# Kernel tuning notes

Measured on AMD Instinct MI355X. Metric: run time of the kernel, lower is better.

The kernel has to match this reference:

```python
import jax, jax.numpy as jnp
import numpy as np

B = 16384
S0, S1 = 7, 7
NB, NC = 2, 20
WC, WN = 5.0, 0.5  # weight_coord, weight_noobject
D = NB * 5 + NC  # 30


def setup_inputs() -> dict:
    key = jax.random.key(0)
    k1, k2, k3, k4 = jax.random.split(key, 4)
    predication = jax.random.normal(k1, (B, S0 * S1 * D), dtype=jnp.float32)
    grid = jax.random.randint(k2, (B, S0, S1), 0, 2, dtype=jnp.int32)
    tbox = jax.random.uniform(k3, (B, S0, S1, 4), dtype=jnp.float32)
    # keep target w,h strictly positive (real boxes), offsets in [0,1)
    tbox = tbox.at[..., 2:].set(0.05 + 0.9 * tbox[..., 2:])
    tcls = jax.random.randint(k4, (B, S0, S1), 0, NC, dtype=jnp.int32)
    return {"predication": predication, "grid": grid, "tbox": tbox, "tcls": tcls}


def _yolo_loss(predication, grid, tbox, tcls):
    pred = predication.reshape(B, S0, S1, D)
    conf = jax.nn.sigmoid(pred[..., :NB])                                  # (B,S0,S1,NB)
    pb = jax.nn.sigmoid(pred[..., NB:5 * NB]).reshape(B, S0, S1, NB, 4)    # (B,S0,S1,NB,4)
    cls = jax.nn.softmax(pred[..., 5 * NB:], axis=-1)                      # (B,S0,S1,NC)

    # cell coordinates: x = column index, y = row index (matches the [1,0] swap in torch code)
    xg = jnp.arange(S1, dtype=pred.dtype)[None, None, :]   # (1,1,S1)
    yg = jnp.arange(S0, dtype=pred.dtype)[None, :, None]   # (1,S0,1)

    tox, toy, tw, th = tbox[..., 0], tbox[..., 1], tbox[..., 2], tbox[..., 3]
    tcx = (xg + tox) / S0
    tcy = (yg + toy) / S1

    pcx = (xg[..., None] + pb[..., 0]) / S0   # (B,S0,S1,NB)
    pcy = (yg[..., None] + pb[..., 1]) / S1
    pw, ph = pb[..., 2], pb[..., 3]

    # IOU of each predicted box vs the cell's target box (same formula as _calc_iou)
    tb_ = jnp.minimum(tcx[..., None] + tw[..., None] / 2, pcx + pw / 2) - \
          jnp.maximum(tcx[..., None] - tw[..., None] / 2, pcx - pw / 2)
    lr_ = jnp.minimum(tcy[..., None] + th[..., None] / 2, pcy + ph / 2) - \
          jnp.maximum(tcy[..., None] - th[..., None] / 2, pcy - ph / 2)
    inter = jnp.where((tb_ < 0) | (lr_ < 0), 0.0, tb_ * lr_)
    iou = inter / ((tw * th)[..., None] + pw * ph - inter)                 # (B,S0,S1,NB)

    # best predictor chosen on detached IOUs (original uses pred_boxes.detach())
    best = jnp.argmax(jax.lax.stop_gradient(iou), axis=-1)                 # (B,S0,S1)

    take = lambda a: jnp.take_along_axis(a, best[..., None], axis=-1)[..., 0]
    iou_b = take(iou)          # attached IOU re-used in confidence loss
    conf_b = take(conf)
    pbb = jnp.take_along_axis(pb, best[..., None, None], axis=3)[..., 0, :]  # (B,S0,S1,4)

    cls_t = jnp.take_along_axis(cls, tcls[..., None], axis=-1)[..., 0]

    coord = (pbb[..., 0] - tox) ** 2 + (pbb[..., 1] - toy) ** 2 \
          + (jnp.sqrt(pbb[..., 2]) - jnp.sqrt(tw)) ** 2 \
          + (jnp.sqrt(pbb[..., 3]) - jnp.sqrt(th)) ** 2

    obj_loss = WC * coord + (conf_b - iou_b) ** 2 + (1.0 - cls_t) ** 2     # (B,S0,S1)
    noobj_loss = WN * jnp.sum(conf ** 2, axis=-1)                          # (B,S0,S1)

    objm = (grid == 1).astype(pred.dtype)
    total = jnp.sum(objm * obj_loss + (1.0 - objm) * noobj_loss)
    return total / B


def reference(predication, grid, tbox, tcls):
    return _yolo_loss(predication, grid, tbox, tcls)
```

## Files before the change

### kernel.cpp

```cpp
#include <hip/hip_runtime.h>
#include <math.h>

namespace {

constexpr int kB    = 16384;
constexpr int kS0   = 7;
constexpr int kS1   = 7;
constexpr int kD    = 30;
constexpr int kCells = kB * kS0 * kS1;
constexpr int TPB   = 256;
constexpr int NBLK  = kCells / TPB;
constexpr float kInv7 = 1.0f / 7.0f;
constexpr float kWC = 5.0f;
constexpr float kWN = 0.5f;

__device__ __forceinline__ float frcp(float x) {
    return __builtin_amdgcn_rcpf(x);
}

__device__ __forceinline__ float sigm(float x) {
    return frcp(1.0f + __expf(-x));
}

__global__ void __launch_bounds__(TPB, 4) yolo_loss_kernel(
    const float* __restrict__ pred,
    const int*   __restrict__ grid,
    const float* __restrict__ tbox,
    const int*   __restrict__ tcls,
    float* __restrict__ partials)
{
    __shared__ float wsum[TPB / 64];

    const int tid  = threadIdx.x;
    const int cell = blockIdx.x * TPB + tid;
    const int wave = tid >> 6;
    const int lane = tid & 63;

    const float2* __restrict__ p2 =
        reinterpret_cast<const float2*>(pred + (size_t)cell * kD);

    float f[kD];
    #pragma unroll
    for (int q = 0; q < kD / 2; ++q) {
        const float2 t = p2[q];
        f[2 * q]     = t.x;
        f[2 * q + 1] = t.y;
    }

    const float4 tb4 = reinterpret_cast<const float4*>(tbox)[cell];
    const int g  = grid[cell];
    const int tc = tcls[cell];

    __builtin_amdgcn_sched_barrier(0);

    const int cj = cell % kS1;
    const int ci = (cell / kS1) % kS0;
    const float tox = tb4.x, toy = tb4.y, tw = tb4.z, th = tb4.w;

    const float conf0 = sigm(f[0]);
    const float conf1 = sigm(f[1]);
    float pbx[2], pby[2], pbw[2], pbh[2];
    #pragma unroll
    for (int k = 0; k < 2; ++k) {
        pbx[k] = sigm(f[2 + 4 * k + 0]);
        pby[k] = sigm(f[2 + 4 * k + 1]);
        pbw[k] = sigm(f[2 + 4 * k + 2]);
        pbh[k] = sigm(f[2 + 4 * k + 3]);
    }

    float csum = 0.0f, et = 0.0f;
    #pragma unroll
    for (int q = 0; q < 20; ++q) {
        const float e = __expf(f[10 + q]);
        csum += e;
        et = (q == tc) ? e : et;
    }
    const float cls_t = et * frcp(csum);

    const float x = (float)cj, y = (float)ci;
    const float tcx = (x + tox) * kInv7;
    const float tcy = (y + toy) * kInv7;
    const float thw = tw * 0.5f, thh = th * 0.5f;
    const float tarea = tw * th;

    float iou[2];
    #pragma unroll
    for (int k = 0; k < 2; ++k) {
        const float pcx = (x + pbx[k]) * kInv7;
        const float pcy = (y + pby[k]) * kInv7;
        const float pw = pbw[k], ph = pbh[k];
        const float tb_ = fminf(tcx + thw, pcx + pw * 0.5f) - fmaxf(tcx - thw, pcx - pw * 0.5f);
        const float lr_ = fminf(tcy + thh, pcy + ph * 0.5f) - fmaxf(tcy - thh, pcy - ph * 0.5f);
        float inter = tb_ * lr_;
        inter = (tb_ < 0.0f || lr_ < 0.0f) ? 0.0f : inter;
        iou[k] = inter * frcp(tarea + pw * ph - inter);
    }

    const bool b1 = (iou[1] > iou[0]);
    const float bx = b1 ? pbx[1] : pbx[0];
    const float by = b1 ? pby[1] : pby[0];
    const float bw = b1 ? pbw[1] : pbw[0];
    const float bh = b1 ? pbh[1] : pbh[0];
    const float conf_b = b1 ? conf1 : conf0;
    const float iou_b  = b1 ? iou[1] : iou[0];

    const float dx = bx - tox;
    const float dy = by - toy;
    const float dw = sqrtf(bw) - sqrtf(tw);
    const float dh = sqrtf(bh) - sqrtf(th);
    const float coord = dx * dx + dy * dy + dw * dw + dh * dh;
    const float d1 = conf_b - iou_b;
    const float d2 = 1.0f - cls_t;
    const float obj   = kWC * coord + d1 * d1 + d2 * d2;
    const float noobj = kWN * (conf0 * conf0 + conf1 * conf1);

    float v = (g == 1) ? obj : noobj;

    #pragma unroll
    for (int off = 32; off > 0; off >>= 1) v += __shfl_down(v, off, 64);
    if (lane == 0) wsum[wave] = v;
    __syncthreads();
    if (tid == 0) {
        partials[blockIdx.x] = wsum[0] + wsum[1] + wsum[2] + wsum[3];
    }
}

__global__ void __launch_bounds__(256) finish_kernel(
    const float* __restrict__ partials, float* __restrict__ out)
{
    __shared__ float wsum[4];
    const int tid = threadIdx.x;
    float v = 0.0f;
    for (int i = tid; i < NBLK; i += 256) v += partials[i];
    #pragma unroll
    for (int off = 32; off > 0; off >>= 1) v += __shfl_down(v, off, 64);
    if ((tid & 63) == 0) wsum[tid >> 6] = v;
    __syncthreads();
    if (tid == 0) out[0] = (wsum[0] + wsum[1] + wsum[2] + wsum[3]) * (1.0f / kB);
}

}

extern "C" void kernel_launch(void* const* d_in, const int* in_sizes, int n_in,
                              void* d_out, int out_size, void* d_ws, size_t ws_size,
                              hipStream_t stream) {
    const float* pred = (const float*)d_in[0];
    const int*   grid = (const int*)d_in[1];
    const float* tbox = (const float*)d_in[2];
    const int*   tcls = (const int*)d_in[3];
    float* out      = (float*)d_out;
    float* partials = (float*)d_ws;

    yolo_loss_kernel<<<NBLK, TPB, 0, stream>>>(pred, grid, tbox, tcls, partials);
    finish_kernel<<<1, 256, 0, stream>>>(partials, out);
}
```

Before: 159.8 us.

## Process four tiles per block with register double-buffered prefetch

Each block now handles four 256-cell tiles instead of one, prefetching the next tile's predictions and targets into a second register buffer while the current tile is computed. This cuts the block count and partial-sum count by four and aims to overlap global-load latency with the math. In exchange, register pressure roughly doubles and occupancy is lowered (launch bounds go from 4 to 3 blocks), which could weaken latency hiding in this memory-bound kernel.

```diff
diff --git a/kernel.cpp b/kernel.cpp
--- a/kernel.cpp
+++ b/kernel.cpp
@@ -9,7 +9,8 @@
 constexpr int kD    = 30;
 constexpr int kCells = kB * kS0 * kS1;
 constexpr int TPB   = 256;
-constexpr int NBLK  = kCells / TPB;
+constexpr int T     = 4;
+constexpr int NBLK  = kCells / (TPB * T);
 constexpr float kInv7 = 1.0f / 7.0f;
 constexpr float kWC = 5.0f;
 constexpr float kWN = 0.5f;
@@ -22,7 +23,7 @@
     return frcp(1.0f + __expf(-x));
 }
 
-__global__ void __launch_bounds__(TPB, 4) yolo_loss_kernel(
+__global__ void __launch_bounds__(TPB, 3) yolo_loss_kernel(
     const float* __restrict__ pred,
     const int*   __restrict__ grid,
     const float* __restrict__ tbox,
@@ -32,89 +33,109 @@
     __shared__ float wsum[TPB / 64];
 
     const int tid  = threadIdx.x;
-    const int cell = blockIdx.x * TPB + tid;
     const int wave = tid >> 6;
     const int lane = tid & 63;
 
-    const float2* __restrict__ p2 =
-        reinterpret_cast<const float2*>(pred + (size_t)cell * kD);
+    float2 r[2][kD / 2];
+    float4 tb[2];
+    int    gg[2], tc[2];
 
-    float f[kD];
+    auto load_tile = [&](int t, int buf) {
+        const int cell = (blockIdx.x * T + t) * TPB + tid;
+        const float2* __restrict__ p2 =
+            reinterpret_cast<const float2*>(pred + (size_t)cell * kD);
+        #pragma unroll
+        for (int q = 0; q < kD / 2; ++q) r[buf][q] = p2[q];
+        tb[buf] = reinterpret_cast<const float4*>(tbox)[cell];
+        gg[buf] = grid[cell];
+        tc[buf] = tcls[cell];
+    };
+
+    auto compute_tile = [&](int t, int buf) -> float {
+        const int cell = (blockIdx.x * T + t) * TPB + tid;
+
+        float f[kD];
+        #pragma unroll
+        for (int q = 0; q < kD / 2; ++q) {
+            f[2 * q]     = r[buf][q].x;
+            f[2 * q + 1] = r[buf][q].y;
+        }
+
+        const int cj = cell % kS1;
+        const int ci = (cell / kS1) % kS0;
+        const float tox = tb[buf].x, toy = tb[buf].y;
+        const float tw  = tb[buf].z, th  = tb[buf].w;
+        const int g2 = gg[buf], tcv = tc[buf];
+
+        const float conf0 = sigm(f[0]);
+        const float conf1 = sigm(f[1]);
+        float pbx[2], pby[2], pbw[2], pbh[2];
+        #pragma unroll
+        for (int k = 0; k < 2; ++k) {
+            pbx[k] = sigm(f[2 + 4 * k + 0]);
+            pby[k] = sigm(f[2 + 4 * k + 1]);
+            pbw[k] = sigm(f[2 + 4 * k + 2]);
+            pbh[k] = sigm(f[2 + 4 * k + 3]);
+        }
+
+        float csum = 0.0f, et = 0.0f;
+        #pragma unroll
+        for (int q = 0; q < 20; ++q) {
+            const float e = __expf(f[10 + q]);
+            csum += e;
+            et = (q == tcv) ? e : et;
+        }
+        const float cls_t = et * frcp(csum);
+
+        const float x = (float)cj, y = (float)ci;
+        const float tcx = (x + tox) * kInv7;
+        const float tcy = (y + toy) * kInv7;
+        const float thw = tw * 0.5f, thh = th * 0.5f;
+        const float tarea = tw * th;
+
+        float iou[2];
+        #pragma unroll
+        for (int k = 0; k < 2; ++k) {
+            const float pcx = (x + pbx[k]) * kInv7;
+            const float pcy = (y + pby[k]) * kInv7;
+            const float pw = pbw[k], ph = pbh[k];
+            const float tb_ = fminf(tcx + thw, pcx + pw * 0.5f) - fmaxf(tcx - thw, pcx - pw * 0.5f);
+            const float lr_ = fminf(tcy + thh, pcy + ph * 0.5f) - fmaxf(tcy - thh, pcy - ph * 0.5f);
+            float inter = tb_ * lr_;
+            inter = (tb_ < 0.0f || lr_ < 0.0f) ? 0.0f : inter;
+            iou[k] = inter * frcp(tarea + pw * ph - inter);
+        }
+
+        const bool b1 = (iou[1] > iou[0]);
+        const float bx = b1 ? pbx[1] : pbx[0];
+        const float by = b1 ? pby[1] : pby[0];
+        const float bw = b1 ? pbw[1] : pbw[0];
+        const float bh = b1 ? pbh[1] : pbh[0];
+        const float conf_b = b1 ? conf1 : conf0;
+        const float iou_b  = b1 ? iou[1] : iou[0];
+
+        const float dx = bx - tox;
+        const float dy = by - toy;
+        const float dw = sqrtf(bw) - sqrtf(tw);
+        const float dh = sqrtf(bh) - sqrtf(th);
+        const float coord = dx * dx + dy * dy + dw * dw + dh * dh;
+        const float d1 = conf_b - iou_b;
+        const float d2 = 1.0f - cls_t;
+        const float obj   = kWC * coord + d1 * d1 + d2 * d2;
+        const float noobj = kWN * (conf0 * conf0 + conf1 * conf1);
+
+        return (g2 == 1) ? obj : noobj;
+    };
+
+    float v = 0.0f;
+    load_tile(0, 0);
     #pragma unroll
-    for (int q = 0; q < kD / 2; ++q) {
-        const float2 t = p2[q];
-        f[2 * q]     = t.x;
-        f[2 * q + 1] = t.y;
+    for (int t = 0; t < T; ++t) {
+        const int cur = t & 1;
+        if (t + 1 < T) load_tile(t + 1, cur ^ 1);
+        __builtin_amdgcn_sched_barrier(0);
+        v += compute_tile(t, cur);
     }
-
-    const float4 tb4 = reinterpret_cast<const float4*>(tbox)[cell];
-    const int g  = grid[cell];
-    const int tc = tcls[cell];
-
-    __builtin_amdgcn_sched_barrier(0);
-
-    const int cj = cell % kS1;
-    const int ci = (cell / kS1) % kS0;
-    const float tox = tb4.x, toy = tb4.y, tw = tb4.z, th = tb4.w;
-
-    const float conf0 = sigm(f[0]);
-    const float conf1 = sigm(f[1]);
-    float pbx[2], pby[2], pbw[2], pbh[2];
-    #pragma unroll
-    for (int k = 0; k < 2; ++k) {
-        pbx[k] = sigm(f[2 + 4 * k + 0]);
-        pby[k] = sigm(f[2 + 4 * k + 1]);
-        pbw[k] = sigm(f[2 + 4 * k + 2]);
-        pbh[k] = sigm(f[2 + 4 * k + 3]);
-    }
-
-    float csum = 0.0f, et = 0.0f;
-    #pragma unroll
-    for (int q = 0; q < 20; ++q) {
-        const float e = __expf(f[10 + q]);
-        csum += e;
-        et = (q == tc) ? e : et;
-    }
-    const float cls_t = et * frcp(csum);
-
-    const float x = (float)cj, y = (float)ci;
-    const float tcx = (x + tox) * kInv7;
-    const float tcy = (y + toy) * kInv7;
-    const float thw = tw * 0.5f, thh = th * 0.5f;
-    const float tarea = tw * th;
-
-    float iou[2];
-    #pragma unroll
-    for (int k = 0; k < 2; ++k) {
-        const float pcx = (x + pbx[k]) * kInv7;
-        const float pcy = (y + pby[k]) * kInv7;
-        const float pw = pbw[k], ph = pbh[k];
-        const float tb_ = fminf(tcx + thw, pcx + pw * 0.5f) - fmaxf(tcx - thw, pcx - pw * 0.5f);
-        const float lr_ = fminf(tcy + thh, pcy + ph * 0.5f) - fmaxf(tcy - thh, pcy - ph * 0.5f);
-        float inter = tb_ * lr_;
-        inter = (tb_ < 0.0f || lr_ < 0.0f) ? 0.0f : inter;
-        iou[k] = inter * frcp(tarea + pw * ph - inter);
-    }
-
-    const bool b1 = (iou[1] > iou[0]);
-    const float bx = b1 ? pbx[1] : pbx[0];
-    const float by = b1 ? pby[1] : pby[0];
-    const float bw = b1 ? pbw[1] : pbw[0];
-    const float bh = b1 ? pbh[1] : pbh[0];
-    const float conf_b = b1 ? conf1 : conf0;
-    const float iou_b  = b1 ? iou[1] : iou[0];
-
-    const float dx = bx - tox;
-    const float dy = by - toy;
-    const float dw = sqrtf(bw) - sqrtf(tw);
-    const float dh = sqrtf(bh) - sqrtf(th);
-    const float coord = dx * dx + dy * dy + dw * dw + dh * dh;
-    const float d1 = conf_b - iou_b;
-    const float d2 = 1.0f - cls_t;
-    const float obj   = kWC * coord + d1 * d1 + d2 * d2;
-    const float noobj = kWN * (conf0 * conf0 + conf1 * conf1);
-
-    float v = (g == 1) ? obj : noobj;
 
     #pragma unroll
     for (int off = 32; off > 0; off >>= 1) v += __shfl_down(v, off, 64);
```

Result: slower. 166.1 us (+3.9%).
